# Optimization experiments

Measured on AMD Instinct MI355X. Metric: run time of the kernel, lower is better.

The kernel has to match this reference:

```python
import jax, jax.numpy as jnp
import numpy as np

N = 50000
E = 600000
OB_DIM = 128
H = 128
P_OUT = 8


def _glorot(key, fan_in, fan_out):
    lim = float(np.sqrt(6.0 / (fan_in + fan_out)))
    return jax.random.uniform(key, (fan_in, fan_out), jnp.float32, -lim, lim)


def setup_inputs() -> dict:
    key = jax.random.key(0)
    ks = jax.random.split(key, 16)
    x = jax.random.normal(ks[0], (N, OB_DIM), jnp.float32)
    edge_index = jax.random.randint(ks[1], (2, E), 0, N, jnp.int64)
    dims = [(OB_DIM, H), (H, H), (H, P_OUT), (OB_DIM, H), (H, H), (H, 1)]
    names = ["p1", "p2", "p3", "v1", "v2", "v3"]
    inp = {"x": x, "edge_index": edge_index}
    for i, (nm, (fi, fo)) in enumerate(zip(names, dims)):
        inp["W" + nm] = _glorot(ks[2 + i], fi, fo)
        inp["b" + nm] = jnp.zeros((fo,), jnp.float32)
    return inp


def _gcn_norm(edge_index, n):
    # add self-loops, symmetric normalization deg^{-1/2} A_hat deg^{-1/2}
    loops = jnp.arange(n, dtype=edge_index.dtype)
    src = jnp.concatenate([edge_index[0], loops])
    dst = jnp.concatenate([edge_index[1], loops])
    deg = jax.ops.segment_sum(jnp.ones_like(dst, jnp.float32), dst, num_segments=n)
    dinv = jax.lax.rsqrt(jnp.maximum(deg, 1.0))
    norm = dinv[src] * dinv[dst]  # [E+N]
    return src, dst, norm


def _gcn_conv(x, W, b, src, dst, norm, n):
    h = x @ W                      # [N, out]
    msg = h[src] * norm[:, None]   # gather + scale, [E+N, out]
    out = jax.ops.segment_sum(msg, dst, num_segments=n)
    return out + b


def reference(x, edge_index, Wp1, bp1, Wp2, bp2, Wp3, bp3, Wv1, bv1, Wv2, bv2, Wv3, bv3):
    n = x.shape[0]
    src, dst, norm = _gcn_norm(edge_index, n)
    # policy branch
    a = jax.nn.relu(_gcn_conv(x, Wp1, bp1, src, dst, norm, n))
    a = jax.nn.relu(_gcn_conv(a, Wp2, bp2, src, dst, norm, n))
    action_logits = _gcn_conv(a, Wp3, bp3, src, dst, norm, n)  # Categorical logits
    # value branch
    v = jax.nn.relu(_gcn_conv(x, Wv1, bv1, src, dst, norm, n))
    v = jax.nn.relu(_gcn_conv(v, Wv2, bv2, src, dst, norm, n))
    v = _gcn_conv(v, Wv3, bv3, src, dst, norm, n)
    return action_logits, v
```

## Files before the change

kernel.cpp:

```cpp
#include <hip/hip_runtime.h>

#define NN 50000
#define NE 600000

typedef unsigned short ushort_t;
typedef ushort_t ushortx8 __attribute__((ext_vector_type(8)));
typedef ushort_t ushortx4 __attribute__((ext_vector_type(4)));
typedef short bf16x8 __attribute__((ext_vector_type(8)));
typedef float f32x4 __attribute__((ext_vector_type(4)));

__device__ __forceinline__ float bf2f(ushort_t u) {
    union { unsigned int i; float f; } c;
    c.i = ((unsigned int)u) << 16;
    return c.f;
}
__device__ __forceinline__ ushort_t f2bf(float f) {
    union { float f; unsigned int i; } c;
    c.f = f;
    unsigned int u = c.i;
    unsigned int r = u + 0x7FFFu + ((u >> 16) & 1u);
    return (ushort_t)(r >> 16);
}
__device__ __forceinline__ unsigned cvtpk(float lo, float hi) {
    unsigned r;
    asm("v_cvt_pk_bf16_f32 %0, %1, %2" : "=v"(r) : "v"(lo), "v"(hi));
    return r;
}


__global__ void k_count(const int* __restrict__ ei, int* __restrict__ cnt) {
    int e = blockIdx.x * 256 + threadIdx.x;
    if (e < NE) atomicAdd(&cnt[ei[NE + e]], 1);
}

__global__ void k_scan1(const int* __restrict__ cnt, int* __restrict__ rowptr,
                        int* __restrict__ bsum, float* __restrict__ dinv) {
    __shared__ int s[256];
    int t = threadIdx.x;
    int i = blockIdx.x * 256 + t;
    int v = (i < NN) ? cnt[i] : 0;
    if (i < NN) dinv[i] = rsqrtf(1.0f + (float)v);
    s[t] = v;
    __syncthreads();
    for (int d = 1; d < 256; d <<= 1) {
        int tmp = (t >= d) ? s[t - d] : 0;
        __syncthreads();
        s[t] += tmp;
        __syncthreads();
    }
    if (i < NN) rowptr[i] = s[t] - v;
    if (t == 255) bsum[blockIdx.x] = s[255];
}

__global__ void k_scan2(int* __restrict__ bsum, int* __restrict__ boff, int nb) {
    __shared__ int s[256];
    int t = threadIdx.x;
    int v = (t < nb) ? bsum[t] : 0;
    s[t] = v;
    __syncthreads();
    for (int d = 1; d < 256; d <<= 1) {
        int tmp = (t >= d) ? s[t - d] : 0;
        __syncthreads();
        s[t] += tmp;
        __syncthreads();
    }
    boff[t] = s[t] - v;
}

__global__ void k_scan3(int* __restrict__ rowptr, const int* __restrict__ boff) {
    int i = blockIdx.x * 256 + threadIdx.x;
    if (i < NN) rowptr[i] += boff[blockIdx.x];
}

__global__ void k_fill(const int* __restrict__ ei, const int* __restrict__ rowptr,
                       int* __restrict__ fill, const float* __restrict__ dinv,
                       int2* __restrict__ edges) {
    int e = blockIdx.x * 256 + threadIdx.x;
    if (e < NE) {
        int s = ei[e];
        int d = ei[NE + e];
        int pos = rowptr[d] + atomicAdd(&fill[d], 1);
        float w = dinv[s] * dinv[d];
        int2 pr;
        pr.x = s;
        pr.y = __float_as_int(w);
        edges[pos] = pr;
    }
}

__global__ void k_prep_w(const float* __restrict__ Wp1, const float* __restrict__ Wv1,
                         const float* __restrict__ Wp2, const float* __restrict__ Wv2,
                         ushort_t* __restrict__ Wt1, ushort_t* __restrict__ Wt2p,
                         ushort_t* __restrict__ Wt2v) {
    int b = blockIdx.x, t = threadIdx.x;
    if (b < 128) {
        int idx = b * 256 + t;
        int n = idx >> 7, k = idx & 127;
        float v = (n < 128) ? Wp1[k * 128 + n] : Wv1[k * 128 + (n - 128)];
        Wt1[n * 128 + k] = f2bf(v);
    } else if (b < 192) {
        int idx = (b - 128) * 256 + t;
        int n = idx >> 7, k = idx & 127;
        Wt2p[n * 128 + k] = f2bf(Wp2[k * 128 + n]);
    } else {
        int idx = (b - 192) * 256 + t;
        int n = idx >> 7, k = idx & 127;
        Wt2v[n * 128 + k] = f2bf(Wv2[k * 128 + n]);
    }
}

__global__ __launch_bounds__(256) void k_gemm1(const float* __restrict__ X,
                                               const ushort_t* __restrict__ Wt1,
                                               ushort_t* __restrict__ C, int nrows) {
    __shared__ ushort_t Wl[256 * 128];
    int t = threadIdx.x;
    const ushortx8* Wg = (const ushortx8*)Wt1;
#pragma unroll
    for (int i = 0; i < 16; ++i) {
        int c = i * 256 + t;
        int row = c >> 4, slot = c & 15;
        int db = row * 256 + ((slot * 16) ^ ((row & 7) << 4));
        *(ushortx8*)((char*)Wl + db) = Wg[c];
    }
    __syncthreads();

    int w = t >> 6, l = t & 63, m = l & 15, g = l >> 4;
    int r0 = blockIdx.x * 64 + w * 16;
    if (r0 >= nrows) return;

    const float* Arow = X + (size_t)(r0 + m) * 128;
    bf16x8 af[4];
#pragma unroll
    for (int kk = 0; kk < 4; ++kk) {
        float4 lo = *(const float4*)(Arow + kk * 32 + g * 8);
        float4 hi = *(const float4*)(Arow + kk * 32 + g * 8 + 4);
        union { unsigned u[4]; bf16x8 v; } cv;
        cv.u[0] = cvtpk(lo.x, lo.y);
        cv.u[1] = cvtpk(lo.z, lo.w);
        cv.u[2] = cvtpk(hi.x, hi.y);
        cv.u[3] = cvtpk(hi.z, hi.w);
        af[kk] = cv.v;
    }

    f32x4 acc[16];
#pragma unroll
    for (int nt = 0; nt < 16; ++nt) acc[nt] = (f32x4){0.f, 0.f, 0.f, 0.f};
    int sw = (m & 7) << 4;
#pragma unroll
    for (int nt = 0; nt < 16; ++nt) {
        const char* Wb = (const char*)Wl + (nt * 16 + m) * 256;
#pragma unroll
        for (int kk = 0; kk < 4; ++kk) {
            bf16x8 wf = *(const bf16x8*)(Wb + ((kk * 64 + g * 16) ^ sw));
            acc[nt] = __builtin_amdgcn_mfma_f32_16x16x32_bf16(wf, af[kk], acc[nt], 0, 0, 0);
        }
    }
#pragma unroll
    for (int nt = 0; nt < 16; ++nt) {
        ushortx4 o = {f2bf(acc[nt][0]), f2bf(acc[nt][1]), f2bf(acc[nt][2]), f2bf(acc[nt][3])};
        *(ushortx4*)(C + (size_t)(r0 + m) * 256 + nt * 16 + g * 4) = o;
    }
}

__global__ __launch_bounds__(256) void k_gemm2(const ushort_t* __restrict__ A,
                                               const ushort_t* __restrict__ Wp,
                                               const ushort_t* __restrict__ Wv,
                                               ushort_t* __restrict__ C, int nrows) {
    __shared__ ushort_t Wl[2 * 128 * 128];
    int t = threadIdx.x;
    const ushortx8* Wgp = (const ushortx8*)Wp;
    const ushortx8* Wgv = (const ushortx8*)Wv;
#pragma unroll
    for (int i = 0; i < 8; ++i) {
        int c = i * 256 + t;
        int row = c >> 4, slot = c & 15;
        int db = row * 256 + ((slot * 16) ^ ((row & 7) << 4));
        *(ushortx8*)((char*)Wl + db) = Wgp[c];
        *(ushortx8*)((char*)Wl + 32768 + db) = Wgv[c];
    }
    __syncthreads();

    int w = t >> 6, l = t & 63, m = l & 15, g = l >> 4;
    int r0 = blockIdx.x * 64 + w * 16;
    if (r0 >= nrows) return;

    const ushort_t* Arow = A + (size_t)(r0 + m) * 256;
    bf16x8 alo[4], ahi[4];
#pragma unroll
    for (int kk = 0; kk < 4; ++kk) {
        alo[kk] = *(const bf16x8*)(Arow + kk * 32 + g * 8);
        ahi[kk] = *(const bf16x8*)(Arow + 128 + kk * 32 + g * 8);
    }

    f32x4 accp[8], accv[8];
#pragma unroll
    for (int nt = 0; nt < 8; ++nt) {
        accp[nt] = (f32x4){0.f, 0.f, 0.f, 0.f};
        accv[nt] = (f32x4){0.f, 0.f, 0.f, 0.f};
    }
    int sw = (m & 7) << 4;
#pragma unroll
    for (int nt = 0; nt < 8; ++nt) {
        const char* Wbp = (const char*)Wl + (nt * 16 + m) * 256;
        const char* Wbv = Wbp + 32768;
#pragma unroll
        for (int kk = 0; kk < 4; ++kk) {
            int off = (kk * 64 + g * 16) ^ sw;
            bf16x8 wfp = *(const bf16x8*)(Wbp + off);
            accp[nt] = __builtin_amdgcn_mfma_f32_16x16x32_bf16(wfp, alo[kk], accp[nt], 0, 0, 0);
            bf16x8 wfv = *(const bf16x8*)(Wbv + off);
            accv[nt] = __builtin_amdgcn_mfma_f32_16x16x32_bf16(wfv, ahi[kk], accv[nt], 0, 0, 0);
        }
    }
#pragma unroll
    for (int nt = 0; nt < 8; ++nt) {
        ushortx4 op = {f2bf(accp[nt][0]), f2bf(accp[nt][1]), f2bf(accp[nt][2]), f2bf(accp[nt][3])};
        ushortx4 ov = {f2bf(accv[nt][0]), f2bf(accv[nt][1]), f2bf(accv[nt][2]), f2bf(accv[nt][3])};
        *(ushortx4*)(C + (size_t)(r0 + m) * 256 + nt * 16 + g * 4) = op;
        *(ushortx4*)(C + (size_t)(r0 + m) * 256 + 128 + nt * 16 + g * 4) = ov;
    }
}

__global__ __launch_bounds__(256) void k_agg256(const ushort_t* __restrict__ H,
                                                ushort_t* __restrict__ OUT,
                                                const float* __restrict__ b_lo,
                                                const float* __restrict__ b_hi,
                                                const float* __restrict__ dinv,
                                                const int* __restrict__ rowptr,
                                                const int* __restrict__ cnt,
                                                const int2* __restrict__ edges) {
    int wv = threadIdx.x >> 6;
    int l = threadIdx.x & 63;
    int i = blockIdx.x * 4 + wv;
    if (i >= NN) return;
    int h = l >> 5, q = l & 31;
    const ushortx8* H8 = (const ushortx8*)H;

    float a0[8] = {}, a1[8] = {};
    float di = dinv[i];
    if (h == 0) {
        float ws = di * di;
        ushortx8 hv = H8[(size_t)i * 32 + q];
#pragma unroll
        for (int k = 0; k < 8; ++k) a0[k] = ws * bf2f(hv[k]);
    }
    int st = rowptr[i];
    int n = cnt[i];
    int j = h;
    for (; j + 6 < n; j += 8) {
        int2 e0 = edges[st + j], e1 = edges[st + j + 2];
        int2 e2 = edges[st + j + 4], e3 = edges[st + j + 6];
        float w0 = __int_as_float(e0.y), w1 = __int_as_float(e1.y);
        float w2 = __int_as_float(e2.y), w3 = __int_as_float(e3.y);
        ushortx8 h0 = H8[(size_t)e0.x * 32 + q];
        ushortx8 h1 = H8[(size_t)e1.x * 32 + q];
        ushortx8 h2 = H8[(size_t)e2.x * 32 + q];
        ushortx8 h3 = H8[(size_t)e3.x * 32 + q];
#pragma unroll
        for (int k = 0; k < 8; ++k) a0[k] += w0 * bf2f(h0[k]);
#pragma unroll
        for (int k = 0; k < 8; ++k) a1[k] += w1 * bf2f(h1[k]);
#pragma unroll
        for (int k = 0; k < 8; ++k) a0[k] += w2 * bf2f(h2[k]);
#pragma unroll
        for (int k = 0; k < 8; ++k) a1[k] += w3 * bf2f(h3[k]);
    }
    for (; j < n; j += 2) {
        int2 e0 = edges[st + j];
        float w0 = __int_as_float(e0.y);
        ushortx8 h0 = H8[(size_t)e0.x * 32 + q];
#pragma unroll
        for (int k = 0; k < 8; ++k) a0[k] += w0 * bf2f(h0[k]);
    }
#pragma unroll
    for (int k = 0; k < 8; ++k) a0[k] += a1[k];
#pragma unroll
    for (int k = 0; k < 8; ++k) a0[k] += __shfl_xor(a0[k], 32, 64);

    if (h == 0) {
        const float* bb = (q < 16) ? (b_lo + q * 8) : (b_hi + (q - 16) * 8);
        float4 b0 = *(const float4*)bb;
        float4 b1 = *(const float4*)(bb + 4);
        float r[8];
        r[0] = fmaxf(a0[0] + b0.x, 0.f); r[1] = fmaxf(a0[1] + b0.y, 0.f);
        r[2] = fmaxf(a0[2] + b0.z, 0.f); r[3] = fmaxf(a0[3] + b0.w, 0.f);
        r[4] = fmaxf(a0[4] + b1.x, 0.f); r[5] = fmaxf(a0[5] + b1.y, 0.f);
        r[6] = fmaxf(a0[6] + b1.z, 0.f); r[7] = fmaxf(a0[7] + b1.w, 0.f);
        ushortx8 o = {f2bf(r[0]), f2bf(r[1]), f2bf(r[2]), f2bf(r[3]),
                      f2bf(r[4]), f2bf(r[5]), f2bf(r[6]), f2bf(r[7])};
        ((ushortx8*)OUT)[(size_t)i * 32 + q] = o;
    }
}

__global__ __launch_bounds__(256) void k_small(const ushort_t* __restrict__ F2,
                                               const float* __restrict__ Wp3,
                                               const float* __restrict__ Wv3,
                                               float* __restrict__ FS) {
    __shared__ float Wp[8 * 128];
    __shared__ float Wv[128];
    int t = threadIdx.x;
    for (int j = t; j < 1024; j += 256) {
        int k = j >> 3, c = j & 7;
        Wp[c * 128 + k] = Wp3[j];
    }
    if (t < 128) Wv[t] = Wv3[t];
    __syncthreads();
    int row = blockIdx.x * 256 + t;
    if (row >= NN) return;
    const ushortx8* F8 = (const ushortx8*)F2;
    size_t base = (size_t)row * 32;
    float acc[9] = {};
#pragma unroll 2
    for (int kc = 0; kc < 16; ++kc) {
        ushortx8 p = F8[base + kc];
        ushortx8 v = F8[base + 16 + kc];
#pragma unroll
        for (int jj = 0; jj < 8; ++jj) {
            float pv = bf2f(p[jj]);
            int k = kc * 8 + jj;
#pragma unroll
            for (int c = 0; c < 8; ++c) acc[c] += pv * Wp[c * 128 + k];
            acc[8] += bf2f(v[jj]) * Wv[k];
        }
    }
    float4* FSo = (float4*)(FS + (size_t)row * 12);
    float4 o0 = {acc[0], acc[1], acc[2], acc[3]};
    float4 o1 = {acc[4], acc[5], acc[6], acc[7]};
    float4 o2 = {acc[8], 0.f, 0.f, 0.f};
    FSo[0] = o0; FSo[1] = o1; FSo[2] = o2;
}

__global__ void k_agg9(const float* __restrict__ FS, float* __restrict__ out_logits,
                       float* __restrict__ out_v, const float* __restrict__ bp3,
                       const float* __restrict__ bv3, const float* __restrict__ dinv,
                       const int* __restrict__ rowptr, const int* __restrict__ cnt,
                       const int2* __restrict__ edges) {
    int i = blockIdx.x * 256 + threadIdx.x;
    if (i >= NN) return;
    float di = dinv[i];
    float w0 = di * di;
    const float4* F = (const float4*)FS;
    size_t b0 = (size_t)i * 3;
    float4 x0 = F[b0], x1 = F[b0 + 1], x2 = F[b0 + 2];
    float a[9];
    a[0] = w0 * x0.x; a[1] = w0 * x0.y; a[2] = w0 * x0.z; a[3] = w0 * x0.w;
    a[4] = w0 * x1.x; a[5] = w0 * x1.y; a[6] = w0 * x1.z; a[7] = w0 * x1.w;
    a[8] = w0 * x2.x;
    int st = rowptr[i];
    int n = cnt[i];
    for (int j = 0; j < n; ++j) {
        int2 e = edges[st + j];
        float w = __int_as_float(e.y);
        size_t sb = (size_t)e.x * 3;
        float4 y0 = F[sb], y1 = F[sb + 1], y2 = F[sb + 2];
        a[0] += w * y0.x; a[1] += w * y0.y; a[2] += w * y0.z; a[3] += w * y0.w;
        a[4] += w * y1.x; a[5] += w * y1.y; a[6] += w * y1.z; a[7] += w * y1.w;
        a[8] += w * y2.x;
    }
    float4 bpa = *(const float4*)bp3;
    float4 bpb = *(const float4*)(bp3 + 4);
    float4 o0 = {a[0] + bpa.x, a[1] + bpa.y, a[2] + bpa.z, a[3] + bpa.w};
    float4 o1 = {a[4] + bpb.x, a[5] + bpb.y, a[6] + bpb.z, a[7] + bpb.w};
    ((float4*)out_logits)[(size_t)i * 2] = o0;
    ((float4*)out_logits)[(size_t)i * 2 + 1] = o1;
    out_v[i] = a[8] + bv3[0];
}

extern "C" void kernel_launch(void* const* d_in, const int* in_sizes, int n_in,
                              void* d_out, int out_size, void* d_ws, size_t ws_size,
                              hipStream_t stream) {
    const float* x   = (const float*)d_in[0];
    const int*   ei  = (const int*)d_in[1];
    const float* Wp1 = (const float*)d_in[2],  *bp1 = (const float*)d_in[3];
    const float* Wp2 = (const float*)d_in[4],  *bp2 = (const float*)d_in[5];
    const float* Wp3 = (const float*)d_in[6],  *bp3 = (const float*)d_in[7];
    const float* Wv1 = (const float*)d_in[8],  *bv1 = (const float*)d_in[9];
    const float* Wv2 = (const float*)d_in[10], *bv2 = (const float*)d_in[11];
    const float* Wv3 = (const float*)d_in[12], *bv3 = (const float*)d_in[13];
    float* out_logits = (float*)d_out;
    float* out_v = (float*)d_out + (size_t)NN * 8;

    char* w = (char*)d_ws;
    auto alloc = [&](size_t bytes) {
        char* p = w;
        w += (bytes + 255) & ~(size_t)255;
        return p;
    };
    int*      cntfill = (int*)alloc((size_t)2 * NN * 4);
    int*      cnt    = cntfill;
    int*      fill   = cntfill + NN;
    int*      rowptr = (int*)alloc(NN * 4);
    int*      bsum   = (int*)alloc(256 * 4);
    int*      boff   = (int*)alloc(256 * 4);
    float*    dinv   = (float*)alloc(NN * 4);
    int2*     edges  = (int2*)alloc((size_t)NE * 8);
    ushort_t* Wt1    = (ushort_t*)alloc(256 * 128 * 2);
    ushort_t* Wt2p   = (ushort_t*)alloc(128 * 128 * 2);
    ushort_t* Wt2v   = (ushort_t*)alloc(128 * 128 * 2);
    ushort_t* Hb     = (ushort_t*)alloc((size_t)NN * 256 * 2);
    ushort_t* f1b    = (ushort_t*)alloc((size_t)NN * 256 * 2);
    ushort_t* f2b    = (ushort_t*)alloc((size_t)NN * 256 * 2);
    float*    fs     = (float*)alloc((size_t)NN * 12 * 4);

    const int NB = (NN + 255) / 256;
    const int EB = (NE + 255) / 256;
    const int GB = (NN + 63) / 64;
    const int AB = NN / 4;

    hipMemsetAsync(cntfill, 0, (size_t)2 * NN * 4, stream);
    k_count<<<EB, 256, 0, stream>>>(ei, cnt);
    k_scan1<<<NB, 256, 0, stream>>>(cnt, rowptr, bsum, dinv);
    k_scan2<<<1, 256, 0, stream>>>(bsum, boff, NB);
    k_scan3<<<NB, 256, 0, stream>>>(rowptr, boff);
    k_fill<<<EB, 256, 0, stream>>>(ei, rowptr, fill, dinv, edges);

    k_prep_w<<<256, 256, 0, stream>>>(Wp1, Wv1, Wp2, Wv2, Wt1, Wt2p, Wt2v);

    k_gemm1<<<GB, 256, 0, stream>>>(x, Wt1, Hb, NN);
    k_agg256<<<AB, 256, 0, stream>>>(Hb, f1b, bp1, bv1, dinv, rowptr, cnt, edges);
    k_gemm2<<<GB, 256, 0, stream>>>(f1b, Wt2p, Wt2v, Hb, NN);
    k_agg256<<<AB, 256, 0, stream>>>(Hb, f2b, bp2, bv2, dinv, rowptr, cnt, edges);
    k_small<<<NB, 256, 0, stream>>>(f2b, Wp3, Wv3, fs);
    k_agg9<<<NB, 256, 0, stream>>>(fs, out_logits, out_v, bp3, bv3, dinv, rowptr, cnt, edges);
}
```

Before: 234.8 us.

## Merge scan and weight-prep kernels, pack rowptr/count, deepen gather batching

Folds the single-block scan into the weight-prep launch, which removes one kernel launch. It also packs rowptr and count into one int2 array so each node needs a single load. The 256-wide aggregation loop now loads 16-byte edge pairs with nontemporal hints and issues eight feature gathers per iteration, masking out-of-range entries with zero weights. This adds memory-level parallelism but does some wasted loads on low-degree rows. Nontemporal loads and stores are also applied to the edge-index reads and the output writes to reduce cache pollution.

Result: slower. 260.3 us (+10.8%).

```diff
diff --git a/kernel.cpp b/kernel.cpp
--- a/kernel.cpp
+++ b/kernel.cpp
@@ -8,6 +8,8 @@
 typedef ushort_t ushortx4 __attribute__((ext_vector_type(4)));
 typedef short bf16x8 __attribute__((ext_vector_type(8)));
 typedef float f32x4 __attribute__((ext_vector_type(4)));
+typedef int intx4 __attribute__((ext_vector_type(4)));
+typedef float fltx4 __attribute__((ext_vector_type(4)));
 
 __device__ __forceinline__ float bf2f(ushort_t u) {
     union { unsigned int i; float f; } c;
@@ -30,7 +32,10 @@
 
 __global__ void k_count(const int* __restrict__ ei, int* __restrict__ cnt) {
     int e = blockIdx.x * 256 + threadIdx.x;
-    if (e < NE) atomicAdd(&cnt[ei[NE + e]], 1);
+    if (e < NE) {
+        int d = __builtin_nontemporal_load(ei + NE + e);
+        atomicAdd(&cnt[d], 1);
+    }
 }
 
 __global__ void k_scan1(const int* __restrict__ cnt, int* __restrict__ rowptr,
@@ -52,46 +57,11 @@
     if (t == 255) bsum[blockIdx.x] = s[255];
 }
 
-__global__ void k_scan2(int* __restrict__ bsum, int* __restrict__ boff, int nb) {
-    __shared__ int s[256];
-    int t = threadIdx.x;
-    int v = (t < nb) ? bsum[t] : 0;
-    s[t] = v;
-    __syncthreads();
-    for (int d = 1; d < 256; d <<= 1) {
-        int tmp = (t >= d) ? s[t - d] : 0;
-        __syncthreads();
-        s[t] += tmp;
-        __syncthreads();
-    }
-    boff[t] = s[t] - v;
-}
-
-__global__ void k_scan3(int* __restrict__ rowptr, const int* __restrict__ boff) {
-    int i = blockIdx.x * 256 + threadIdx.x;
-    if (i < NN) rowptr[i] += boff[blockIdx.x];
-}
-
-__global__ void k_fill(const int* __restrict__ ei, const int* __restrict__ rowptr,
-                       int* __restrict__ fill, const float* __restrict__ dinv,
-                       int2* __restrict__ edges) {
-    int e = blockIdx.x * 256 + threadIdx.x;
-    if (e < NE) {
-        int s = ei[e];
-        int d = ei[NE + e];
-        int pos = rowptr[d] + atomicAdd(&fill[d], 1);
-        float w = dinv[s] * dinv[d];
-        int2 pr;
-        pr.x = s;
-        pr.y = __float_as_int(w);
-        edges[pos] = pr;
-    }
-}
-
-__global__ void k_prep_w(const float* __restrict__ Wp1, const float* __restrict__ Wv1,
-                         const float* __restrict__ Wp2, const float* __restrict__ Wv2,
-                         ushort_t* __restrict__ Wt1, ushort_t* __restrict__ Wt2p,
-                         ushort_t* __restrict__ Wt2v) {
+__global__ void k_scan2_prep(int* __restrict__ bsum, int* __restrict__ boff, int nb,
+                             const float* __restrict__ Wp1, const float* __restrict__ Wv1,
+                             const float* __restrict__ Wp2, const float* __restrict__ Wv2,
+                             ushort_t* __restrict__ Wt1, ushort_t* __restrict__ Wt2p,
+                             ushort_t* __restrict__ Wt2v) {
     int b = blockIdx.x, t = threadIdx.x;
     if (b < 128) {
         int idx = b * 256 + t;
@@ -102,10 +72,48 @@
         int idx = (b - 128) * 256 + t;
         int n = idx >> 7, k = idx & 127;
         Wt2p[n * 128 + k] = f2bf(Wp2[k * 128 + n]);
-    } else {
+    } else if (b < 256) {
         int idx = (b - 192) * 256 + t;
         int n = idx >> 7, k = idx & 127;
         Wt2v[n * 128 + k] = f2bf(Wv2[k * 128 + n]);
+    } else {
+        __shared__ int s[256];
+        int v = (t < nb) ? bsum[t] : 0;
+        s[t] = v;
+        __syncthreads();
+        for (int d = 1; d < 256; d <<= 1) {
+            int tmp = (t >= d) ? s[t - d] : 0;
+            __syncthreads();
+            s[t] += tmp;
+            __syncthreads();
+        }
+        boff[t] = s[t] - v;
+    }
+}
+
+__global__ void k_scan3rc(const int* __restrict__ rowptr, const int* __restrict__ cnt,
+                          const int* __restrict__ boff, int2* __restrict__ rc) {
+    int i = blockIdx.x * 256 + threadIdx.x;
+    if (i < NN) {
+        int2 v;
+        v.x = rowptr[i] + boff[blockIdx.x];
+        v.y = cnt[i];
+        rc[i] = v;
+    }
+}
+
+__global__ void k_fill(const int* __restrict__ ei, const int2* __restrict__ rc,
+                       int* __restrict__ fill, const float* __restrict__ dinv,
+                       int2* __restrict__ edges) {
+    int e = blockIdx.x * 256 + threadIdx.x;
+    if (e < NE) {
+        int s = __builtin_nontemporal_load(ei + e);
+        int d = __builtin_nontemporal_load(ei + NE + e);
+        int pos = rc[d].x + atomicAdd(&fill[d], 1);
+        int2 pr;
+        pr.x = s;
+        pr.y = __float_as_int(dinv[s] * dinv[d]);
+        edges[pos] = pr;
     }
 }
 
@@ -226,8 +234,7 @@
                                                 const float* __restrict__ b_lo,
                                                 const float* __restrict__ b_hi,
                                                 const float* __restrict__ dinv,
-                                                const int* __restrict__ rowptr,
-                                                const int* __restrict__ cnt,
+                                                const int2* __restrict__ rc,
                                                 const int2* __restrict__ edges) {
     int wv = threadIdx.x >> 6;
     int l = threadIdx.x & 63;
@@ -244,33 +251,32 @@
 #pragma unroll
         for (int k = 0; k < 8; ++k) a0[k] = ws * bf2f(hv[k]);
     }
-    int st = rowptr[i];
-    int n = cnt[i];
-    int j = h;
-    for (; j + 6 < n; j += 8) {
-        int2 e0 = edges[st + j], e1 = edges[st + j + 2];
-        int2 e2 = edges[st + j + 4], e3 = edges[st + j + 6];
-        float w0 = __int_as_float(e0.y), w1 = __int_as_float(e1.y);
-        float w2 = __int_as_float(e2.y), w3 = __int_as_float(e3.y);
-        ushortx8 h0 = H8[(size_t)e0.x * 32 + q];
-        ushortx8 h1 = H8[(size_t)e1.x * 32 + q];
-        ushortx8 h2 = H8[(size_t)e2.x * 32 + q];
-        ushortx8 h3 = H8[(size_t)e3.x * 32 + q];
-#pragma unroll
-        for (int k = 0; k < 8; ++k) a0[k] += w0 * bf2f(h0[k]);
-#pragma unroll
-        for (int k = 0; k < 8; ++k) a1[k] += w1 * bf2f(h1[k]);
-#pragma unroll
-        for (int k = 0; k < 8; ++k) a0[k] += w2 * bf2f(h2[k]);
-#pragma unroll
-        for (int k = 0; k < 8; ++k) a1[k] += w3 * bf2f(h3[k]);
-    }
-    for (; j < n; j += 2) {
-        int2 e0 = edges[st + j];
-        float w0 = __int_as_float(e0.y);
-        ushortx8 h0 = H8[(size_t)e0.x * 32 + q];
-#pragma unroll
-        for (int k = 0; k < 8; ++k) a0[k] += w0 * bf2f(h0[k]);
+    int2 rcv = rc[i];
+    int st = rcv.x, n = rcv.y;
+
+    for (int j = h; j < n; j += 16) {
+        int jb = st + (j - h);
+        float w[8];
+        int idx[8];
+#pragma unroll
+        for (int s = 0; s < 8; ++s) {
+            int jj = j + 2 * s;
+            int ea = jb + 2 * s;
+            ea = (ea > NE - 2) ? (NE - 2) : ea;
+            intx4 em = __builtin_nontemporal_load((const intx4*)(edges + ea));
+            idx[s] = h ? em.z : em.x;
+            int wz = h ? em.w : em.y;
+            w[s] = (jj < n) ? __int_as_float(wz) : 0.f;
+        }
+        ushortx8 hh[8];
+#pragma unroll
+        for (int s = 0; s < 8; ++s) hh[s] = H8[(size_t)idx[s] * 32 + q];
+#pragma unroll
+        for (int s = 0; s < 8; ++s) {
+            float* a = (s & 1) ? a1 : a0;
+#pragma unroll
+            for (int k = 0; k < 8; ++k) a[k] += w[s] * bf2f(hh[s][k]);
+        }
     }
 #pragma unroll
     for (int k = 0; k < 8; ++k) a0[k] += a1[k];
@@ -288,7 +294,7 @@
         r[6] = fmaxf(a0[6] + b1.z, 0.f); r[7] = fmaxf(a0[7] + b1.w, 0.f);
         ushortx8 o = {f2bf(r[0]), f2bf(r[1]), f2bf(r[2]), f2bf(r[3]),
                       f2bf(r[4]), f2bf(r[5]), f2bf(r[6]), f2bf(r[7])};
-        ((ushortx8*)OUT)[(size_t)i * 32 + q] = o;
+        __builtin_nontemporal_store(o, (ushortx8*)OUT + (size_t)i * 32 + q);
     }
 }
 
@@ -333,8 +339,7 @@
 __global__ void k_agg9(const float* __restrict__ FS, float* __restrict__ out_logits,
                        float* __restrict__ out_v, const float* __restrict__ bp3,
                        const float* __restrict__ bv3, const float* __restrict__ dinv,
-                       const int* __restrict__ rowptr, const int* __restrict__ cnt,
-                       const int2* __restrict__ edges) {
+                       const int2* __restrict__ rc, const int2* __restrict__ edges) {
     int i = blockIdx.x * 256 + threadIdx.x;
     if (i >= NN) return;
     float di = dinv[i];
@@ -346,8 +351,8 @@
     a[0] = w0 * x0.x; a[1] = w0 * x0.y; a[2] = w0 * x0.z; a[3] = w0 * x0.w;
     a[4] = w0 * x1.x; a[5] = w0 * x1.y; a[6] = w0 * x1.z; a[7] = w0 * x1.w;
     a[8] = w0 * x2.x;
-    int st = rowptr[i];
-    int n = cnt[i];
+    int2 rcv = rc[i];
+    int st = rcv.x, n = rcv.y;
     for (int j = 0; j < n; ++j) {
         int2 e = edges[st + j];
         float w = __int_as_float(e.y);
@@ -359,11 +364,11 @@
     }
     float4 bpa = *(const float4*)bp3;
     float4 bpb = *(const float4*)(bp3 + 4);
-    float4 o0 = {a[0] + bpa.x, a[1] + bpa.y, a[2] + bpa.z, a[3] + bpa.w};
-    float4 o1 = {a[4] + bpb.x, a[5] + bpb.y, a[6] + bpb.z, a[7] + bpb.w};
-    ((float4*)out_logits)[(size_t)i * 2] = o0;
-    ((float4*)out_logits)[(size_t)i * 2 + 1] = o1;
-    out_v[i] = a[8] + bv3[0];
+    fltx4 o0 = {a[0] + bpa.x, a[1] + bpa.y, a[2] + bpa.z, a[3] + bpa.w};
+    fltx4 o1 = {a[4] + bpb.x, a[5] + bpb.y, a[6] + bpb.z, a[7] + bpb.w};
+    __builtin_nontemporal_store(o0, (fltx4*)out_logits + (size_t)i * 2);
+    __builtin_nontemporal_store(o1, (fltx4*)out_logits + (size_t)i * 2 + 1);
+    __builtin_nontemporal_store(a[8] + bv3[0], out_v + i);
 }
 
 extern "C" void kernel_launch(void* const* d_in, const int* in_sizes, int n_in,
@@ -393,6 +398,7 @@
     int*      bsum   = (int*)alloc(256 * 4);
     int*      boff   = (int*)alloc(256 * 4);
     float*    dinv   = (float*)alloc(NN * 4);
+    int2*     rc     = (int2*)alloc((size_t)NN * 8);
     int2*     edges  = (int2*)alloc((size_t)NE * 8);
     ushort_t* Wt1    = (ushort_t*)alloc(256 * 128 * 2);
     ushort_t* Wt2p   = (ushort_t*)alloc(128 * 128 * 2);
@@ -407,19 +413,18 @@
     const int GB = (NN + 63) / 64;
     const int AB = NN / 4;
 
-    hipMemsetAsync(cntfill, 0, (size_t)2 * NN * 4, stream);
+    (void)hipMemsetAsync(cntfill, 0, (size_t)2 * NN * 4, stream);
     k_count<<<EB, 256, 0, stream>>>(ei, cnt);
     k_scan1<<<NB, 256, 0, stream>>>(cnt, rowptr, bsum, dinv);
-    k_scan2<<<1, 256, 0, stream>>>(bsum, boff, NB);
-    k_scan3<<<NB, 256, 0, stream>>>(rowptr, boff);
-    k_fill<<<EB, 256, 0, stream>>>(ei, rowptr, fill, dinv, edges);
-
-    k_prep_w<<<256, 256, 0, stream>>>(Wp1, Wv1, Wp2, Wv2, Wt1, Wt2p, Wt2v);
+    k_scan2_prep<<<257, 256, 0, stream>>>(bsum, boff, NB, Wp1, Wv1, Wp2, Wv2,
+                                          Wt1, Wt2p, Wt2v);
+    k_scan3rc<<<NB, 256, 0, stream>>>(rowptr, cnt, boff, rc);
+    k_fill<<<EB, 256, 0, stream>>>(ei, rc, fill, dinv, edges);
 
     k_gemm1<<<GB, 256, 0, stream>>>(x, Wt1, Hb, NN);
-    k_agg256<<<AB, 256, 0, stream>>>(Hb, f1b, bp1, bv1, dinv, rowptr, cnt, edges);
+    k_agg256<<<AB, 256, 0, stream>>>(Hb, f1b, bp1, bv1, dinv, rc, edges);
     k_gemm2<<<GB, 256, 0, stream>>>(f1b, Wt2p, Wt2v, Hb, NN);
-    k_agg256<<<AB, 256, 0, stream>>>(Hb, f2b, bp2, bv2, dinv, rowptr, cnt, edges);
+    k_agg256<<<AB, 256, 0, stream>>>(Hb, f2b, bp2, bv2, dinv, rc, edges);
     k_small<<<NB, 256, 0, stream>>>(f2b, Wp3, Wv3, fs);
-    k_agg9<<<NB, 256, 0, stream>>>(fs, out_logits, out_v, bp3, bv3, dinv, rowptr, cnt, edges);
-}
+    k_agg9<<<NB, 256, 0, stream>>>(fs, out_logits, out_v, bp3, bv3, dinv, rc, edges);
+}
```
